# Kernel optimization log

Measured on AMD Instinct MI355X. Metric: run time of the kernel, lower is better.

Reference implementation:

```python
import jax, jax.numpy as jnp
import numpy as np


def gru_cell(inp, h, wi, wh, bi, bh):
    # torch nn.GRU cell math: gates ordered (r, z, n)
    gi = inp @ wi.T + bi          # [3H]
    gh = h @ wh.T + bh            # [3H]
    ir, iz, inn = jnp.split(gi, 3, axis=-1)
    hr, hz, hn = jnp.split(gh, 3, axis=-1)
    r = jax.nn.sigmoid(ir + hr)
    z = jax.nn.sigmoid(iz + hz)
    n = jnp.tanh(inn + r * hn)
    return (1.0 - z) * n + z * h


def setup_inputs() -> dict:
    key = jax.random.key(0)
    C, L = 1024, 2048  # input_size / hidden_size, sequence length
    ks = jax.random.split(key, 11)
    x = jax.random.normal(ks[0], (1, L, C), jnp.float32)
    # attention: Linear(2C, 1), weight ~ N(0, 0.01), bias = -1 (per module init)
    attn_w = jax.random.normal(ks[1], (1, 2 * C), jnp.float32) * 0.01
    attn_b = jnp.full((1,), -1.0, jnp.float32)
    # GRU default torch init: U(-1/sqrt(H), 1/sqrt(H))
    s = 1.0 / np.sqrt(C).astype(np.float32)
    u = lambda k, shape: jax.random.uniform(k, shape, jnp.float32, -s, s)
    w_ih0 = u(ks[2], (3 * C, C)); w_hh0 = u(ks[3], (3 * C, C))
    b_ih0 = u(ks[4], (3 * C,));   b_hh0 = u(ks[5], (3 * C,))
    w_ih1 = u(ks[6], (3 * C, C)); w_hh1 = u(ks[7], (3 * C, C))
    b_ih1 = u(ks[8], (3 * C,));   b_hh1 = u(ks[9], (3 * C,))
    return {"x": x, "attn_w": attn_w, "attn_b": attn_b,
            "w_ih0": w_ih0, "w_hh0": w_hh0, "b_ih0": b_ih0, "b_hh0": b_hh0,
            "w_ih1": w_ih1, "w_hh1": w_hh1, "b_ih1": b_ih1, "b_hh1": b_hh1,
            "lengths": L}


def reference(x, attn_w, attn_b, w_ih0, w_hh0, b_ih0, b_hh0,
              w_ih1, w_hh1, b_ih1, b_hh1, lengths):
    x0 = x[0]                     # [L, C]; batch must be 1
    L, C = x0.shape
    dt = x.dtype

    def step(carry, _):
        out, h0, h1 = carry       # out: [C], h0/h1: [C]
        # attention: score each timestep against previous output
        concated = jnp.concatenate(
            [jnp.broadcast_to(out, (L, C)), x0], axis=1)  # [L, 2C]
        logits = concated @ attn_w.T + attn_b             # [L, 1]
        a = jax.nn.softmax(logits, axis=0)                # softmax over L
        av = jnp.sum(a * x0, axis=0)                      # [C] context vector
        # 2-layer GRU, one timestep
        h0n = gru_cell(av, h0, w_ih0, w_hh0, b_ih0, b_hh0)
        h1n = gru_cell(h0n, h1, w_ih1, w_hh1, b_ih1, b_hh1)
        return (h1n, h0n, h1n), h1n

    init = (jnp.zeros((C,), dt), jnp.zeros((C,), dt), jnp.zeros((C,), dt))
    (_, h0, h1), outs = jax.lax.scan(step, init, None, length=lengths)
    outputs = outs[None]                                  # [1, L, C]
    previous_state = jnp.stack([h0, h1])[:, None, :]      # [2, 1, C]
    return outputs, previous_state
```

## Files before the change

kernel.cpp:

```cpp
#include <hip/hip_runtime.h>
#include <math.h>

#define CC 1024
#define LL 2048
#define NWG 256
#define NT 256

typedef float f4 __attribute__((ext_vector_type(4)));
typedef unsigned u4 __attribute__((ext_vector_type(4)));

#define PKT_PAR 4096
#define PKT_ARR 1024
#define WS_FLAGS 8192
#define WS_REL 16384
#define WS_LOGITS 16448
#define WS_AV (WS_LOGITS + LL)
#define WS_MEMSET_BYTES ((WS_REL + 64) * 4)

__device__ __forceinline__ float aload(const float* p) {
  return __hip_atomic_load(p, __ATOMIC_RELAXED, __HIP_MEMORY_SCOPE_AGENT);
}
__device__ __forceinline__ void astore(float* p, float v) {
  __hip_atomic_store(p, v, __ATOMIC_RELAXED, __HIP_MEMORY_SCOPE_AGENT);
}
__device__ __forceinline__ float sigm(float x) { return 1.0f / (1.0f + __expf(-x)); }
__device__ __forceinline__ float tanh_(float x) { return 2.0f / (1.0f + __expf(-2.0f * x)) - 1.0f; }

__device__ __forceinline__ float dot4(f4 a, f4 b) {
  return fmaf(a.x, b.x, fmaf(a.y, b.y, fmaf(a.z, b.z, a.w * b.w)));
}

__device__ __forceinline__ u4 ld16v(const unsigned* p) {
  u4 r;
  asm volatile("global_load_dwordx4 %0, %1, off sc0 sc1" : "=v"(r) : "v"(p) : "memory");
  return r;
}
__device__ __forceinline__ void vm0() { asm volatile("s_waitcnt vmcnt(0)" ::: "memory"); }
__device__ __forceinline__ void st16u(unsigned* p, u4 v) {
  asm volatile("global_store_dwordx4 %0, %1, off sc0 sc1" ::"v"(p), "v"(v) : "memory");
}

__device__ __forceinline__ void gbar(unsigned* ws_u, unsigned epoch) {
  __syncthreads();
  if (blockIdx.x == 0) {
    const int i = threadIdx.x;
    if (i > 0 && i < NWG) {
      unsigned* slot = ws_u + WS_FLAGS + i * 32;
      while (__hip_atomic_load(slot, __ATOMIC_RELAXED, __HIP_MEMORY_SCOPE_AGENT) < epoch) {
      }
      (void)__hip_atomic_load(slot, __ATOMIC_ACQUIRE, __HIP_MEMORY_SCOPE_AGENT);
    }
    __syncthreads();
    if (i == 0)
      __hip_atomic_store(ws_u + WS_REL, epoch, __ATOMIC_RELEASE, __HIP_MEMORY_SCOPE_AGENT);
    __syncthreads();
  } else {
    if (threadIdx.x == 0) {
      __hip_atomic_store(ws_u + WS_FLAGS + blockIdx.x * 32, epoch, __ATOMIC_RELEASE,
                         __HIP_MEMORY_SCOPE_AGENT);
      unsigned* rel = ws_u + WS_REL;
      while (__hip_atomic_load(rel, __ATOMIC_RELAXED, __HIP_MEMORY_SCOPE_AGENT) < epoch) {
      }
      (void)__hip_atomic_load(rel, __ATOMIC_ACQUIRE, __HIP_MEMORY_SCOPE_AGENT);
    }
    __syncthreads();
  }
}

__global__ __launch_bounds__(NT, 1) void decoder_kernel(
    const float* __restrict__ x, const float* __restrict__ attn_w,
    const float* __restrict__ w_ih0, const float* __restrict__ w_hh0,
    const float* __restrict__ b_ih0, const float* __restrict__ b_hh0,
    const float* __restrict__ w_ih1, const float* __restrict__ w_hh1,
    const float* __restrict__ b_ih1, const float* __restrict__ b_hh1,
    float* __restrict__ out, float* __restrict__ ws) {
  const int g = blockIdx.x;
  const int tid = threadIdx.x;
  const int lane = tid & 63;
  const int w = tid >> 6;
  const int eg = 4 * g + w;

  unsigned* ws_u = (unsigned*)ws;

  extern __shared__ float wlds[];
  __shared__ __align__(16) float h0s[CC];
  __shared__ __align__(16) float h1s[CC];
  __shared__ float cgi0[12], cbh0[12], cbh1[12], cbi1[12];
  __shared__ float red[NT];

  {
    const float* w2 = attn_w + CC;
#pragma unroll
    for (int s = 0; s < 2; ++s) {
      int t = 8 * g + 2 * w + s;
      const float* xr = x + (size_t)t * CC;
      float p = 0.f;
#pragma unroll
      for (int k = 0; k < 4; ++k) {
        f4 xa = *(const f4*)(xr + 256 * k + 4 * lane);
        f4 wa = *(const f4*)(w2 + 256 * k + 4 * lane);
        p += dot4(xa, wa);
      }
#pragma unroll
      for (int off = 32; off; off >>= 1) p += __shfl_xor(p, off, 64);
      if (lane == 0) astore(ws + WS_LOGITS + t, p);
    }
  }
  gbar(ws_u, 1);

  {
    float myl[8];
#pragma unroll
    for (int s = 0; s < 8; ++s) myl[s] = aload(ws + WS_LOGITS + tid + 256 * s);
    float lm = myl[0];
#pragma unroll
    for (int s = 1; s < 8; ++s) lm = fmaxf(lm, myl[s]);
    red[tid] = lm;
    __syncthreads();
    for (int stp = 128; stp; stp >>= 1) {
      if (tid < stp) red[tid] = fmaxf(red[tid], red[tid + stp]);
      __syncthreads();
    }
    float m = red[0];
    __syncthreads();
    float myw[8];
    float ls = 0.f;
#pragma unroll
    for (int s = 0; s < 8; ++s) {
      myw[s] = __expf(myl[s] - m);
      ls += myw[s];
    }
    red[tid] = ls;
    __syncthreads();
    for (int stp = 128; stp; stp >>= 1) {
      if (tid < stp) red[tid] += red[tid + stp];
      __syncthreads();
    }
    float invZ = 1.0f / red[0];
    __syncthreads();
    float acc[4] = {0.f, 0.f, 0.f, 0.f};
#pragma unroll
    for (int s = 0; s < 8; ++s) {
      int t = tid + 256 * s;
      f4 xa = *(const f4*)(x + (size_t)t * CC + 4 * g);
      acc[0] = fmaf(myw[s], xa.x, acc[0]);
      acc[1] = fmaf(myw[s], xa.y, acc[1]);
      acc[2] = fmaf(myw[s], xa.z, acc[2]);
      acc[3] = fmaf(myw[s], xa.w, acc[3]);
    }
    for (int i = 0; i < 4; ++i) {
      red[tid] = acc[i];
      __syncthreads();
      for (int stp = 128; stp; stp >>= 1) {
        if (tid < stp) red[tid] += red[tid + stp];
        __syncthreads();
      }
      if (tid == 0) astore(ws + WS_AV + 4 * g + i, red[0] * invZ);
      __syncthreads();
    }
  }
  gbar(ws_u, 2);

#pragma unroll
  for (int i = 0; i < 4; ++i) h0s[4 * tid + i] = aload(ws + WS_AV + 4 * tid + i);
  __syncthreads();
  {
    f4 hc[4];
#pragma unroll
    for (int k = 0; k < 4; ++k) hc[k] = *(const f4*)&h0s[256 * k + 4 * lane];
#pragma unroll
    for (int jj = 0; jj < 3; ++jj) {
      int j = 3 * w + jj;
      int gate = j >> 2, e = j & 3;
      int row = gate * CC + 4 * g + e;
      const float* wr = w_ih0 + (size_t)row * CC;
      float p = 0.f;
#pragma unroll
      for (int k = 0; k < 4; ++k) p += dot4(*(const f4*)(wr + 256 * k + 4 * lane), hc[k]);
#pragma unroll
      for (int off = 32; off; off >>= 1) p += __shfl_xor(p, off, 64);
      if (lane == 0) cgi0[j] = p + b_ih0[row];
    }
  }
  if (tid < 12) {
    int gate = tid >> 2, e = tid & 3;
    int row = gate * CC + 4 * g + e;
    cbh0[tid] = b_hh0[row];
    cbh1[tid] = b_hh1[row];
    cbi1[tid] = b_ih1[row];
  }

#pragma unroll
  for (int j = 0; j < 36; ++j) {
    int ww = j / 9, r = j % 9, mat = r / 3, G = r % 3;
    const float* src = (mat == 0 ? w_hh0 : (mat == 1 ? w_hh1 : w_ih1)) +
                       ((size_t)(G * CC + 4 * g + ww) << 10);
    *(f4*)&wlds[j * 1024 + 4 * tid] = *(const f4*)(src + 4 * tid);
  }
#pragma unroll
  for (int i = 0; i < 4; ++i) {
    h0s[4 * tid + i] = 0.f;
    h1s[4 * tid + i] = 0.f;
  }
  __syncthreads();

  float h0last = 0.f;
  unsigned* pkt0 = ws_u;
  unsigned* pkt1 = ws_u + PKT_PAR;
  u4 qa, qb, qc, qd;
  const float* wr9 = wlds + (w * 9) * 1024;

  for (int tau = 0; tau <= LL; ++tau) {
    if (tau > 0) {
      const unsigned ut = (unsigned)tau;
      unsigned* base = (tau & 1) ? pkt1 : pkt0;
      const unsigned* pA = base + 0 * PKT_ARR + 4 * tid;
      const unsigned* pB = base + 1 * PKT_ARR + 4 * tid;
      const unsigned* pC = base + 2 * PKT_ARR + 4 * tid;
      const unsigned* pD = base + 3 * PKT_ARR + 4 * tid;
      vm0();
      while (qa.w != ut || qb.w != ut || qc.w != ut || qd.w != ut) {
        qa = ld16v(pA);
        qb = ld16v(pB);
        qc = ld16v(pC);
        qd = ld16v(pD);
        vm0();
      }
      f4 v0, v1;
      v0.x = __uint_as_float(qa.x);
      v0.y = __uint_as_float(qb.x);
      v0.z = __uint_as_float(qc.x);
      v0.w = __uint_as_float(qd.x);
      v1.x = __uint_as_float(qa.y);
      v1.y = __uint_as_float(qb.y);
      v1.z = __uint_as_float(qc.y);
      v1.w = __uint_as_float(qd.y);
      *(f4*)&h0s[4 * tid] = v0;
      *(f4*)&h1s[4 * tid] = v1;
    }
    __syncthreads();
    f4 hc0[4], hc1[4];
#pragma unroll
    for (int k = 0; k < 4; ++k) {
      hc0[k] = *(const f4*)&h0s[256 * k + 4 * lane];
      hc1[k] = *(const f4*)&h1s[256 * k + 4 * lane];
    }
    float h0prev = h0s[eg];
    float h1prev = h1s[eg];
    float p[9];
#pragma unroll
    for (int G = 0; G < 3; ++G) {
      float pa = 0.f, pb = 0.f, pc = 0.f;
#pragma unroll
      for (int k = 0; k < 4; ++k) {
        int off = 256 * k + 4 * lane;
        pa += dot4(*(const f4*)&wr9[(0 * 3 + G) * 1024 + off], hc0[k]);
        pb += dot4(*(const f4*)&wr9[(1 * 3 + G) * 1024 + off], hc1[k]);
        pc += dot4(*(const f4*)&wr9[(2 * 3 + G) * 1024 + off], hc0[k]);
      }
      p[G] = pa;
      p[3 + G] = pb;
      p[6 + G] = pc;
    }
#pragma unroll
    for (int off = 32; off; off >>= 1) {
#pragma unroll
      for (int i = 0; i < 9; ++i) p[i] += __shfl_xor(p[i], off, 64);
    }
    float r0 = sigm(cgi0[w] + p[0] + cbh0[w]);
    float z0 = sigm(cgi0[4 + w] + p[1] + cbh0[4 + w]);
    float n0 = tanh_(cgi0[8 + w] + r0 * (p[2] + cbh0[8 + w]));
    float h0new = (1.f - z0) * n0 + z0 * h0prev;

    float r1 = sigm(p[6] + cbi1[w] + p[3] + cbh1[w]);
    float z1 = sigm(p[7] + cbi1[4 + w] + p[4] + cbh1[4 + w]);
    float n1 = tanh_(p[8] + cbi1[8 + w] + r1 * (p[5] + cbh1[8 + w]));
    float h1new = (1.f - z1) * n1 + z1 * h1prev;

    if (lane == 0) {
      if (tau < LL) {
        u4 pk;
        pk.x = __float_as_uint(h0new);
        pk.y = __float_as_uint((tau > 0) ? h1new : 0.f);
        pk.z = 0u;
        pk.w = (unsigned)(tau + 1);
        unsigned* dst = (((tau + 1) & 1) ? pkt1 : pkt0) + w * PKT_ARR + 4 * g;
        st16u(dst, pk);
      }
      if (tau > 0) out[(size_t)(tau - 1) * CC + eg] = h1new;
      if (tau == LL) {
        out[(size_t)LL * CC + eg] = h0last;
        out[(size_t)LL * CC + CC + eg] = h1new;
      }
    }
    if (tau == LL - 1) h0last = h0new;
    if (tau < LL) {
      unsigned* nb = ((tau + 1) & 1) ? pkt1 : pkt0;
      qa = ld16v(nb + 0 * PKT_ARR + 4 * tid);
      qb = ld16v(nb + 1 * PKT_ARR + 4 * tid);
      qc = ld16v(nb + 2 * PKT_ARR + 4 * tid);
      qd = ld16v(nb + 3 * PKT_ARR + 4 * tid);
    }
    __syncthreads();
  }
}

extern "C" void kernel_launch(void* const* d_in, const int* in_sizes, int n_in,
                              void* d_out, int out_size, void* d_ws, size_t ws_size,
                              hipStream_t stream) {
  const float* x = (const float*)d_in[0];
  const float* attn_w = (const float*)d_in[1];
  const float* w_ih0 = (const float*)d_in[3];
  const float* w_hh0 = (const float*)d_in[4];
  const float* b_ih0 = (const float*)d_in[5];
  const float* b_hh0 = (const float*)d_in[6];
  const float* w_ih1 = (const float*)d_in[7];
  const float* w_hh1 = (const float*)d_in[8];
  const float* b_ih1 = (const float*)d_in[9];
  const float* b_hh1 = (const float*)d_in[10];
  float* out = (float*)d_out;
  float* ws = (float*)d_ws;

  static int attr_set = 0;
  if (!attr_set) {
    hipFuncSetAttribute((const void*)decoder_kernel,
                        hipFuncAttributeMaxDynamicSharedMemorySize, 36 * 1024 * 4);
    attr_set = 1;
  }

  hipMemsetAsync(d_ws, 0, WS_MEMSET_BYTES, stream);

  void* args[] = {&x,     &attn_w, &w_ih0, &w_hh0, &b_ih0, &b_hh0,
                  &w_ih1, &w_hh1,  &b_ih1, &b_hh1, &out,   &ws};
  hipLaunchCooperativeKernel((void*)decoder_kernel, dim3(NWG), dim3(NT), args,
                             36 * 1024 * 4, stream);
}
```

Measured before the change: 8.512 ms.

## Split h0/h1 exchange into separate packets and keep w_hh0 in registers

```diff
diff --git a/kernel.cpp b/kernel.cpp
--- a/kernel.cpp
+++ b/kernel.cpp
@@ -8,9 +8,10 @@
 
 typedef float f4 __attribute__((ext_vector_type(4)));
 typedef unsigned u4 __attribute__((ext_vector_type(4)));
-
-#define PKT_PAR 4096
-#define PKT_ARR 1024
+typedef unsigned u2v __attribute__((ext_vector_type(2)));
+
+#define H1_BASE 4096
+#define PKT_PAR 2048
 #define WS_FLAGS 8192
 #define WS_REL 16384
 #define WS_LOGITS 16448
@@ -25,7 +26,6 @@
 }
 __device__ __forceinline__ float sigm(float x) { return 1.0f / (1.0f + __expf(-x)); }
 __device__ __forceinline__ float tanh_(float x) { return 2.0f / (1.0f + __expf(-2.0f * x)) - 1.0f; }
-
 __device__ __forceinline__ float dot4(f4 a, f4 b) {
   return fmaf(a.x, b.x, fmaf(a.y, b.y, fmaf(a.z, b.z, a.w * b.w)));
 }
@@ -36,8 +36,8 @@
   return r;
 }
 __device__ __forceinline__ void vm0() { asm volatile("s_waitcnt vmcnt(0)" ::: "memory"); }
-__device__ __forceinline__ void st16u(unsigned* p, u4 v) {
-  asm volatile("global_store_dwordx4 %0, %1, off sc0 sc1" ::"v"(p), "v"(v) : "memory");
+__device__ __forceinline__ void st8u(unsigned* p, u2v v) {
+  asm volatile("global_store_dwordx2 %0, %1, off sc0 sc1" ::"v"(p), "v"(v) : "memory");
 }
 
 __device__ __forceinline__ void gbar(unsigned* ws_u, unsigned epoch) {
@@ -66,6 +66,11 @@
     __syncthreads();
   }
 }
+
+#define PIN12                                                                        \
+  asm volatile("" : "+v"(Wa[0]), "+v"(Wa[1]), "+v"(Wa[2]), "+v"(Wa[3]), "+v"(Wa[4]), \
+                    "+v"(Wa[5]), "+v"(Wa[6]), "+v"(Wa[7]), "+v"(Wa[8]), "+v"(Wa[9]), \
+                    "+v"(Wa[10]), "+v"(Wa[11]))
 
 __global__ __launch_bounds__(NT, 1) void decoder_kernel(
     const float* __restrict__ x, const float* __restrict__ attn_w,
@@ -82,7 +87,7 @@
 
   unsigned* ws_u = (unsigned*)ws;
 
-  extern __shared__ float wlds[];
+  extern __shared__ float wcb[];
   __shared__ __align__(16) float h0s[CC];
   __shared__ __align__(16) float h1s[CC];
   __shared__ float cgi0[12], cbh0[12], cbh1[12], cbi1[12];
@@ -190,12 +195,20 @@
     cbi1[tid] = b_ih1[row];
   }
 
-#pragma unroll
-  for (int j = 0; j < 36; ++j) {
-    int ww = j / 9, r = j % 9, mat = r / 3, G = r % 3;
-    const float* src = (mat == 0 ? w_hh0 : (mat == 1 ? w_hh1 : w_ih1)) +
-                       ((size_t)(G * CC + 4 * g + ww) << 10);
-    *(f4*)&wlds[j * 1024 + 4 * tid] = *(const f4*)(src + 4 * tid);
+  f4 Wa[12];
+#pragma unroll
+  for (int G = 0; G < 3; ++G) {
+    const float* wr = w_hh0 + ((size_t)(G * CC + eg) << 10);
+#pragma unroll
+    for (int k = 0; k < 4; ++k) Wa[G * 4 + k] = *(const f4*)(wr + 256 * k + 4 * lane);
+  }
+
+#pragma unroll
+  for (int j = 0; j < 24; ++j) {
+    int ww = j / 6, r = j % 6;
+    int G = r % 3;
+    const float* src = (r < 3 ? w_ih1 : w_hh1) + ((size_t)(G * CC + 4 * g + ww) << 10);
+    *(f4*)&wcb[(j << 10) + 4 * tid] = *(const f4*)(src + 4 * tid);
   }
 #pragma unroll
   for (int i = 0; i < 4; ++i) {
@@ -205,101 +218,135 @@
   __syncthreads();
 
   float h0last = 0.f;
-  unsigned* pkt0 = ws_u;
-  unsigned* pkt1 = ws_u + PKT_PAR;
-  u4 qa, qb, qc, qd;
-  const float* wr9 = wlds + (w * 9) * 1024;
+  u4 pd0a, pd0b, pd1a, pd1b;
+  const float* wr6 = wcb + (w * 6) * 1024;
 
   for (int tau = 0; tau <= LL; ++tau) {
+    PIN12;
     if (tau > 0) {
       const unsigned ut = (unsigned)tau;
-      unsigned* base = (tau & 1) ? pkt1 : pkt0;
-      const unsigned* pA = base + 0 * PKT_ARR + 4 * tid;
-      const unsigned* pB = base + 1 * PKT_ARR + 4 * tid;
-      const unsigned* pC = base + 2 * PKT_ARR + 4 * tid;
-      const unsigned* pD = base + 3 * PKT_ARR + 4 * tid;
+      const unsigned* p0 = ws_u + (tau & 1) * PKT_PAR + 8 * tid;
       vm0();
-      while (qa.w != ut || qb.w != ut || qc.w != ut || qd.w != ut) {
-        qa = ld16v(pA);
-        qb = ld16v(pB);
-        qc = ld16v(pC);
-        qd = ld16v(pD);
+      while (pd0a.y != ut || pd0a.w != ut || pd0b.y != ut || pd0b.w != ut) {
+        pd0a = ld16v(p0);
+        pd0b = ld16v(p0 + 4);
         vm0();
       }
-      f4 v0, v1;
-      v0.x = __uint_as_float(qa.x);
-      v0.y = __uint_as_float(qb.x);
-      v0.z = __uint_as_float(qc.x);
-      v0.w = __uint_as_float(qd.x);
-      v1.x = __uint_as_float(qa.y);
-      v1.y = __uint_as_float(qb.y);
-      v1.z = __uint_as_float(qc.y);
-      v1.w = __uint_as_float(qd.y);
-      *(f4*)&h0s[4 * tid] = v0;
-      *(f4*)&h1s[4 * tid] = v1;
-    }
-    __syncthreads();
-    f4 hc0[4], hc1[4];
-#pragma unroll
-    for (int k = 0; k < 4; ++k) {
-      hc0[k] = *(const f4*)&h0s[256 * k + 4 * lane];
-      hc1[k] = *(const f4*)&h1s[256 * k + 4 * lane];
-    }
-    float h0prev = h0s[eg];
-    float h1prev = h1s[eg];
-    float p[9];
-#pragma unroll
-    for (int G = 0; G < 3; ++G) {
-      float pa = 0.f, pb = 0.f, pc = 0.f;
+      h0s[4 * tid + 0] = __uint_as_float(pd0a.x);
+      h0s[4 * tid + 1] = __uint_as_float(pd0a.z);
+      h0s[4 * tid + 2] = __uint_as_float(pd0b.x);
+      h0s[4 * tid + 3] = __uint_as_float(pd0b.z);
+      const unsigned* p1 = ws_u + H1_BASE + (tau & 1) * PKT_PAR + 8 * tid;
+      pd1a = ld16v(p1);
+      pd1b = ld16v(p1 + 4);
+    }
+    __syncthreads();
+
+    float h0new = 0.f;
+    if (tau < LL) {
+      f4 hc0[4];
+#pragma unroll
+      for (int k = 0; k < 4; ++k) hc0[k] = *(const f4*)&h0s[256 * k + 4 * lane];
+      float pA[3];
+#pragma unroll
+      for (int G = 0; G < 3; ++G) {
+        float p = 0.f;
+#pragma unroll
+        for (int k = 0; k < 4; ++k) p += dot4(Wa[G * 4 + k], hc0[k]);
+        pA[G] = p;
+      }
+#pragma unroll
+      for (int off = 32; off; off >>= 1) {
+#pragma unroll
+        for (int i = 0; i < 3; ++i) pA[i] += __shfl_xor(pA[i], off, 64);
+      }
+      float h0prev = h0s[eg];
+      float r0 = sigm(cgi0[w] + pA[0] + cbh0[w]);
+      float z0 = sigm(cgi0[4 + w] + pA[1] + cbh0[4 + w]);
+      float n0 = tanh_(cgi0[8 + w] + r0 * (pA[2] + cbh0[8 + w]));
+      h0new = (1.f - z0) * n0 + z0 * h0prev;
+      if (tau == LL - 1) h0last = h0new;
+      if (lane == 0) {
+        u2v pk;
+        pk.x = __float_as_uint(h0new);
+        pk.y = (unsigned)(tau + 1);
+        st8u(ws_u + ((tau + 1) & 1) * PKT_PAR + 2 * eg, pk);
+      }
+    }
+
+    if (tau > 0) {
+      const unsigned ut = (unsigned)tau;
+      const unsigned* p1 = ws_u + H1_BASE + (tau & 1) * PKT_PAR + 8 * tid;
+      vm0();
+      while (pd1a.y != ut || pd1a.w != ut || pd1b.y != ut || pd1b.w != ut) {
+        pd1a = ld16v(p1);
+        pd1b = ld16v(p1 + 4);
+        vm0();
+      }
+      h1s[4 * tid + 0] = __uint_as_float(pd1a.x);
+      h1s[4 * tid + 1] = __uint_as_float(pd1a.z);
+      h1s[4 * tid + 2] = __uint_as_float(pd1b.x);
+      h1s[4 * tid + 3] = __uint_as_float(pd1b.z);
+    }
+    __syncthreads();
+
+    if (tau >= 1) {
+      f4 hc0[4], hc1[4];
 #pragma unroll
       for (int k = 0; k < 4; ++k) {
-        int off = 256 * k + 4 * lane;
-        pa += dot4(*(const f4*)&wr9[(0 * 3 + G) * 1024 + off], hc0[k]);
-        pb += dot4(*(const f4*)&wr9[(1 * 3 + G) * 1024 + off], hc1[k]);
-        pc += dot4(*(const f4*)&wr9[(2 * 3 + G) * 1024 + off], hc0[k]);
-      }
-      p[G] = pa;
-      p[3 + G] = pb;
-      p[6 + G] = pc;
-    }
-#pragma unroll
-    for (int off = 32; off; off >>= 1) {
-#pragma unroll
-      for (int i = 0; i < 9; ++i) p[i] += __shfl_xor(p[i], off, 64);
-    }
-    float r0 = sigm(cgi0[w] + p[0] + cbh0[w]);
-    float z0 = sigm(cgi0[4 + w] + p[1] + cbh0[4 + w]);
-    float n0 = tanh_(cgi0[8 + w] + r0 * (p[2] + cbh0[8 + w]));
-    float h0new = (1.f - z0) * n0 + z0 * h0prev;
-
-    float r1 = sigm(p[6] + cbi1[w] + p[3] + cbh1[w]);
-    float z1 = sigm(p[7] + cbi1[4 + w] + p[4] + cbh1[4 + w]);
-    float n1 = tanh_(p[8] + cbi1[8 + w] + r1 * (p[5] + cbh1[8 + w]));
-    float h1new = (1.f - z1) * n1 + z1 * h1prev;
-
-    if (lane == 0) {
-      if (tau < LL) {
-        u4 pk;
-        pk.x = __float_as_uint(h0new);
-        pk.y = __float_as_uint((tau > 0) ? h1new : 0.f);
-        pk.z = 0u;
-        pk.w = (unsigned)(tau + 1);
-        unsigned* dst = (((tau + 1) & 1) ? pkt1 : pkt0) + w * PKT_ARR + 4 * g;
-        st16u(dst, pk);
-      }
-      if (tau > 0) out[(size_t)(tau - 1) * CC + eg] = h1new;
-      if (tau == LL) {
-        out[(size_t)LL * CC + eg] = h0last;
-        out[(size_t)LL * CC + CC + eg] = h1new;
-      }
-    }
-    if (tau == LL - 1) h0last = h0new;
+        hc0[k] = *(const f4*)&h0s[256 * k + 4 * lane];
+        hc1[k] = *(const f4*)&h1s[256 * k + 4 * lane];
+      }
+      float pC[3], pB[3];
+#pragma unroll
+      for (int G = 0; G < 3; ++G) {
+        float pc = 0.f, pb = 0.f;
+#pragma unroll
+        for (int k = 0; k < 4; ++k) {
+          int off = 256 * k + 4 * lane;
+          pc += dot4(*(const f4*)&wr6[G * 1024 + off], hc0[k]);
+          pb += dot4(*(const f4*)&wr6[(3 + G) * 1024 + off], hc1[k]);
+        }
+        pC[G] = pc;
+        pB[G] = pb;
+      }
+#pragma unroll
+      for (int off = 32; off; off >>= 1) {
+#pragma unroll
+        for (int i = 0; i < 3; ++i) {
+          pC[i] += __shfl_xor(pC[i], off, 64);
+          pB[i] += __shfl_xor(pB[i], off, 64);
+        }
+      }
+      float h1prev = h1s[eg];
+      float r1 = sigm(pC[0] + cbi1[w] + pB[0] + cbh1[w]);
+      float z1 = sigm(pC[1] + cbi1[4 + w] + pB[1] + cbh1[4 + w]);
+      float n1 = tanh_(pC[2] + cbi1[8 + w] + r1 * (pB[2] + cbh1[8 + w]));
+      float h1new = (1.f - z1) * n1 + z1 * h1prev;
+      if (lane == 0) {
+        if (tau < LL) {
+          u2v pk;
+          pk.x = __float_as_uint(h1new);
+          pk.y = (unsigned)(tau + 1);
+          st8u(ws_u + H1_BASE + ((tau + 1) & 1) * PKT_PAR + 2 * eg, pk);
+        }
+        out[(size_t)(tau - 1) * CC + eg] = h1new;
+        if (tau == LL) {
+          out[(size_t)LL * CC + eg] = h0last;
+          out[(size_t)LL * CC + CC + eg] = h1new;
+        }
+      }
+    } else if (lane == 0) {
+      u2v pk;
+      pk.x = 0u;
+      pk.y = 1u;
+      st8u(ws_u + H1_BASE + 1 * PKT_PAR + 2 * eg, pk);
+    }
+
     if (tau < LL) {
-      unsigned* nb = ((tau + 1) & 1) ? pkt1 : pkt0;
-      qa = ld16v(nb + 0 * PKT_ARR + 4 * tid);
-      qb = ld16v(nb + 1 * PKT_ARR + 4 * tid);
-      qc = ld16v(nb + 2 * PKT_ARR + 4 * tid);
-      qd = ld16v(nb + 3 * PKT_ARR + 4 * tid);
+      const unsigned* np = ws_u + ((tau + 1) & 1) * PKT_PAR + 8 * tid;
+      pd0a = ld16v(np);
+      pd0b = ld16v(np + 4);
     }
     __syncthreads();
   }
@@ -324,7 +371,7 @@
   static int attr_set = 0;
   if (!attr_set) {
     hipFuncSetAttribute((const void*)decoder_kernel,
-                        hipFuncAttributeMaxDynamicSharedMemorySize, 36 * 1024 * 4);
+                        hipFuncAttributeMaxDynamicSharedMemorySize, 24 * 1024 * 4);
     attr_set = 1;
   }
 
@@ -333,5 +380,5 @@
   void* args[] = {&x,     &attn_w, &w_ih0, &w_hh0, &b_ih0, &b_hh0,
                   &w_ih1, &w_hh1,  &b_ih1, &b_hh1, &out,   &ws};
   hipLaunchCooperativeKernel((void*)decoder_kernel, dim3(NWG), dim3(NT), args,
-                             36 * 1024 * 4, stream);
-}
+                             24 * 1024 * 4, stream);
+}
```

Measured after the change: 7.336 ms. -13.8%, faster.
